# Optimization experiments

Hardware: AMD Instinct MI355X
Metric: run time of the kernel (lower is better)

Reference implementation:

```python
import jax, jax.numpy as jnp
import numpy as np

MAX_HOPS = 2
N_NODES = 100000
N_EDGES = 1600000
D_FEAT = 64

def setup_inputs() -> dict:
    key = jax.random.key(0)
    k1, k2 = jax.random.split(key)
    x = jax.random.normal(k1, (N_NODES, D_FEAT), dtype=jnp.float32)
    edge_index = jax.random.randint(k2, (2, N_EDGES), 0, N_NODES, dtype=jnp.int64)
    hop_weights = jnp.ones((MAX_HOPS + 1,), dtype=jnp.float32)
    return {"x": x, "edge_index": edge_index, "hop_weights": hop_weights}

def reference(x, edge_index, hop_weights):
    num_nodes = x.shape[0]
    loops = jnp.arange(num_nodes, dtype=edge_index.dtype)
    row = jnp.concatenate([edge_index[0], loops])  # destination of scatter-add
    col = jnp.concatenate([edge_index[1], loops])  # gather source
    # symmetric GCN normalization D^{-1/2} A D^{-1/2} (degree computed over col, as in source)
    deg = jax.ops.segment_sum(jnp.ones_like(col, dtype=x.dtype), col, num_segments=num_nodes)
    deg_inv_sqrt = jnp.where(deg > 0, jax.lax.rsqrt(deg), 0.0)
    norm = deg_inv_sqrt[row] * deg_inv_sqrt[col]  # [E+N]
    w = jax.nn.softmax(hop_weights)
    result = w[0] * x
    current = x
    for hop in range(1, MAX_HOPS + 1):
        messages = current[col] * norm[:, None]  # irregular gather + scale
        current = jax.ops.segment_sum(messages, row, num_segments=num_nodes)  # scatter-add
        result = result + w[hop] * current
    return result
```

## Files before the change

### kernel.cpp

```cpp
#include <hip/hip_runtime.h>

#define NN 100000
#define NE 1600000
#define D 64

#define BKT 256
#define BROWS ((NN + BKT - 1) / BKT)
#define CAP 8192
#define PADCAP 8192
#define P1_NB 512
#define P1_T 1024
#define EPB ((NE + P1_NB - 1) / P1_NB)

typedef unsigned short u16;
typedef unsigned int u32;
typedef unsigned char u8;
typedef __attribute__((ext_vector_type(8))) unsigned short us8;


__device__ __forceinline__ float bf2f(u16 u) {
    union { u32 i; float f; } x; x.i = ((u32)u) << 16; return x.f;
}
__device__ __forceinline__ u16 f2bf(float f) {
    union { float f; u32 i; } x; x.f = f;
    u32 r = x.i + 0x7FFF + ((x.i >> 16) & 1);
    return (u16)(r >> 16);
}

__global__ void softmax_kernel(const float* __restrict__ hw, float* __restrict__ wsm) {
    float m = fmaxf(fmaxf(hw[0], hw[1]), hw[2]);
    float e0 = expf(hw[0] - m), e1 = expf(hw[1] - m), e2 = expf(hw[2] - m);
    float s = e0 + e1 + e2;
    wsm[0] = e0 / s; wsm[1] = e1 / s; wsm[2] = e2 / s;
}

__global__ void __launch_bounds__(P1_T) fused_p1(const int* __restrict__ row,
                                                 const int* __restrict__ col,
                                                 int* __restrict__ bcnt,
                                                 int* __restrict__ bcnt2,
                                                 u32* __restrict__ buck,
                                                 u16* __restrict__ buck2) {
    __shared__ int lds_r[EPB];
    __shared__ int lds_c[EPB];
    __shared__ u32 st1[EPB];
    __shared__ u16 st2[EPB];
    __shared__ u8  sb1[EPB];
    __shared__ u8  sb2[EPB];
    __shared__ int h[BKT], h2[BKT];
    __shared__ int hoff[BKT], hoff2[BKT];
    __shared__ int resv[BKT], resv2[BKT];
    int t = threadIdx.x;
    int beg = blockIdx.x * EPB, end = min(NE, beg + EPB);
    int n = end - beg;
    for (int i = t; i < BKT; i += P1_T) { h[i] = 0; h2[i] = 0; }
    __syncthreads();
    for (int i = t; i < n; i += P1_T) {
        int r = row[beg + i], c = col[beg + i];
        lds_r[i] = r; lds_c[i] = c;
        atomicAdd(&h[r / BROWS], 1);
        atomicAdd(&h2[c / BROWS], 1);
    }
    __syncthreads();
    int id = t & 255;
    int side = t >> 8;
    int* arr = (side == 0) ? h : h2;
    int myc = (side < 2) ? arr[id] : 0;
    for (int st = 1; st < BKT; st <<= 1) {
        int u = 0;
        if (side < 2 && id >= st) u = arr[id - st];
        __syncthreads();
        if (side < 2) arr[id] += u;
        __syncthreads();
    }
    if (side == 0) {
        hoff[id] = h[id] - myc;
        resv[id] = atomicAdd(&bcnt[id], myc);
    } else if (side == 1) {
        hoff2[id] = h2[id] - myc;
        resv2[id] = atomicAdd(&bcnt2[id], myc);
    }
    __syncthreads();
    if (t < BKT) h[t] = hoff[t];
    else if (t < 2 * BKT) h2[t - BKT] = hoff2[t - BKT];
    __syncthreads();
    for (int i = t; i < n; i += P1_T) {
        int r = lds_r[i], c = lds_c[i];
        int b1 = r / BROWS;
        int pos = atomicAdd(&h[b1], 1);
        st1[pos] = ((u32)(r - b1 * BROWS) << 17) | (u32)c;
        sb1[pos] = (u8)b1;
        int b2 = c / BROWS;
        int pos2 = atomicAdd(&h2[b2], 1);
        st2[pos2] = (u16)(c - b2 * BROWS);
        sb2[pos2] = (u8)b2;
    }
    __syncthreads();
    for (int i = t; i < n; i += P1_T) {
        int b1 = sb1[i];
        buck[(size_t)b1 * CAP + resv[b1] + (i - hoff[b1])] = st1[i];
        int b2 = sb2[i];
        buck2[(size_t)b2 * CAP + resv2[b2] + (i - hoff2[b2])] = st2[i];
    }
}

__global__ void __launch_bounds__(1024) deg_count(const int* __restrict__ bcnt2,
                                                  const u16* __restrict__ buck2,
                                                  float* __restrict__ dis,
                                                  float* __restrict__ dsi) {
    __shared__ int ca[BROWS];
    int b = blockIdx.x, t = threadIdx.x;
    int row0 = b * BROWS;
    int nrows = min(BROWS, NN - row0);
    int cntb = bcnt2[b];
    const u16* eb = buck2 + (size_t)b * CAP;
    for (int i = t; i < nrows; i += 1024) ca[i] = 0;
    __syncthreads();
    for (int e = t; e < cntb; e += 1024)
        atomicAdd(&ca[eb[e]], 1);
    __syncthreads();
    if (t < nrows) {
        float dg = (float)(ca[t] + 1);
        dis[row0 + t] = rsqrtf(dg);
        dsi[row0 + t] = sqrtf(dg);
    }
}

__global__ void scale_kernel(const float4* __restrict__ x, const float* __restrict__ dis,
                             ushort4* __restrict__ y1, ushort4* __restrict__ y2) {
    int idx = blockIdx.x * blockDim.x + threadIdx.x;
    if (idx >= (NN + 1) * (D / 4)) return;
    if (idx >= NN * (D / 4)) {
        ushort4 z = {0, 0, 0, 0};
        y1[idx] = z; y2[idx] = z;
        return;
    }
    float s = dis[idx >> 4];
    float4 v = x[idx];
    ushort4 o;
    o.x = f2bf(s * v.x); o.y = f2bf(s * v.y); o.z = f2bf(s * v.z); o.w = f2bf(s * v.w);
    y1[idx] = o;
}

__global__ void __launch_bounds__(1024) p2_build(const int* __restrict__ bcnt,
                                                 const u32* __restrict__ buck,
                                                 int* __restrict__ adjc,
                                                 int2* __restrict__ rowbe) {
    __shared__ int ca[BROWS];
    __shared__ int wsum[16];
    int b = blockIdx.x, t = threadIdx.x;
    int row0 = b * BROWS;
    int nrows = min(BROWS, NN - row0);
    int cntb = bcnt[b];
    const u32* eb = buck + (size_t)b * CAP;

    for (int i = t; i < nrows; i += 1024) ca[i] = 0;
    __syncthreads();
    for (int e = t; e < cntb; e += 1024)
        atomicAdd(&ca[eb[e] >> 17], 1);
    __syncthreads();
    int v = (t < nrows) ? ca[t] : 0;
    int vp = (v + 3) & ~3;
    int lane = t & 63, wv = t >> 6;
    int incl = vp;
    #pragma unroll
    for (int d = 1; d < 64; d <<= 1) {
        int u = __shfl_up(incl, d);
        if (lane >= d) incl += u;
    }
    if (lane == 63) wsum[wv] = incl;
    __syncthreads();
    if (t < 16) {
        int s = wsum[t];
        #pragma unroll
        for (int d = 1; d < 16; d <<= 1) {
            int u = __shfl_up(s, d, 16);
            if (t >= d) s += u;
        }
        wsum[t] = s;
    }
    __syncthreads();
    int excl = ((wv > 0) ? wsum[wv - 1] : 0) + incl - vp;
    if (t < nrows) {
        int base = b * PADCAP + excl;
        rowbe[row0 + t] = make_int2(base, base + vp);
        for (int p = base + v; p < base + vp; ++p) adjc[p] = NN;
        ca[t] = base;
    }
    __syncthreads();
    for (int e = t; e < cntb; e += 1024) {
        u32 p = eb[e];
        int pos = atomicAdd(&ca[p >> 17], 1);
        adjc[pos] = (int)(p & 0x1FFFFu);
    }
}


__global__ void prop1_kernel(const int2* __restrict__ rowbe,
                             const int* __restrict__ adjc,
                             const float* __restrict__ dis,
                             const u16* __restrict__ y1,
                             u16* __restrict__ y2) {
    int tid = blockIdx.x * blockDim.x + threadIdx.x;
    int w = tid >> 6, l = tid & 63;
    int half = l >> 5;
    int n = 2 * w + half;
    int sg = (l >> 3) & 3;
    int ho = l & 7;
    int2 be = rowbe[n];
    int j = be.x, end = be.y;
    float a[8] = {0.f, 0.f, 0.f, 0.f, 0.f, 0.f, 0.f, 0.f};
    while (j + 32 <= end) {
        int4 c0 = *(const int4*)&adjc[j + sg * 4];
        int4 c1 = *(const int4*)&adjc[j + 16 + sg * 4];
        us8 v0 = *(const us8*)&y1[c0.x * D + ho * 8];
        us8 v1 = *(const us8*)&y1[c0.y * D + ho * 8];
        us8 v2 = *(const us8*)&y1[c0.z * D + ho * 8];
        us8 v3 = *(const us8*)&y1[c0.w * D + ho * 8];
        us8 v4 = *(const us8*)&y1[c1.x * D + ho * 8];
        us8 v5 = *(const us8*)&y1[c1.y * D + ho * 8];
        us8 v6 = *(const us8*)&y1[c1.z * D + ho * 8];
        us8 v7 = *(const us8*)&y1[c1.w * D + ho * 8];
        #pragma unroll
        for (int k = 0; k < 8; ++k)
            a[k] += ((bf2f(v0[k]) + bf2f(v1[k])) + (bf2f(v2[k]) + bf2f(v3[k])))
                  + ((bf2f(v4[k]) + bf2f(v5[k])) + (bf2f(v6[k]) + bf2f(v7[k])));
        j += 32;
    }
    if (j + 16 <= end) {
        int4 c0 = *(const int4*)&adjc[j + sg * 4];
        us8 v0 = *(const us8*)&y1[c0.x * D + ho * 8];
        us8 v1 = *(const us8*)&y1[c0.y * D + ho * 8];
        us8 v2 = *(const us8*)&y1[c0.z * D + ho * 8];
        us8 v3 = *(const us8*)&y1[c0.w * D + ho * 8];
        #pragma unroll
        for (int k = 0; k < 8; ++k)
            a[k] += (bf2f(v0[k]) + bf2f(v1[k])) + (bf2f(v2[k]) + bf2f(v3[k]));
        j += 16;
    }
    while (j + 4 <= end) {
        int c = adjc[j + sg];
        us8 v0 = *(const us8*)&y1[c * D + ho * 8];
        #pragma unroll
        for (int k = 0; k < 8; ++k) a[k] += bf2f(v0[k]);
        j += 4;
    }
    #pragma unroll
    for (int k = 0; k < 8; ++k) {
        a[k] += __shfl_xor(a[k], 8);
        a[k] += __shfl_xor(a[k], 16);
    }
    if ((l & 31) < 8) {
        us8 s = *(const us8*)&y1[n * D + ho * 8];
        float di = dis[n], d2 = di * di;
        us8 o;
        #pragma unroll
        for (int k = 0; k < 8; ++k) o[k] = f2bf(d2 * (a[k] + bf2f(s[k])));
        *(us8*)&y2[n * D + ho * 8] = o;
    }
}

__global__ void prop2_kernel(const float* __restrict__ x,
                             const int2* __restrict__ rowbe,
                             const int* __restrict__ adjc,
                             const float* __restrict__ dis,
                             const float* __restrict__ dsi,
                             const u16* __restrict__ y2,
                             const float* __restrict__ wsm,
                             float* __restrict__ out) {
    int tid = blockIdx.x * blockDim.x + threadIdx.x;
    int w = tid >> 6, l = tid & 63;
    int half = l >> 5;
    int n = 2 * w + half;
    int sg = (l >> 3) & 3;
    int ho = l & 7;
    int2 be = rowbe[n];
    int j = be.x, end = be.y;
    float a[8] = {0.f, 0.f, 0.f, 0.f, 0.f, 0.f, 0.f, 0.f};
    while (j + 32 <= end) {
        int4 c0 = *(const int4*)&adjc[j + sg * 4];
        int4 c1 = *(const int4*)&adjc[j + 16 + sg * 4];
        us8 v0 = *(const us8*)&y2[c0.x * D + ho * 8];
        us8 v1 = *(const us8*)&y2[c0.y * D + ho * 8];
        us8 v2 = *(const us8*)&y2[c0.z * D + ho * 8];
        us8 v3 = *(const us8*)&y2[c0.w * D + ho * 8];
        us8 v4 = *(const us8*)&y2[c1.x * D + ho * 8];
        us8 v5 = *(const us8*)&y2[c1.y * D + ho * 8];
        us8 v6 = *(const us8*)&y2[c1.z * D + ho * 8];
        us8 v7 = *(const us8*)&y2[c1.w * D + ho * 8];
        #pragma unroll
        for (int k = 0; k < 8; ++k)
            a[k] += ((bf2f(v0[k]) + bf2f(v1[k])) + (bf2f(v2[k]) + bf2f(v3[k])))
                  + ((bf2f(v4[k]) + bf2f(v5[k])) + (bf2f(v6[k]) + bf2f(v7[k])));
        j += 32;
    }
    if (j + 16 <= end) {
        int4 c0 = *(const int4*)&adjc[j + sg * 4];
        us8 v0 = *(const us8*)&y2[c0.x * D + ho * 8];
        us8 v1 = *(const us8*)&y2[c0.y * D + ho * 8];
        us8 v2 = *(const us8*)&y2[c0.z * D + ho * 8];
        us8 v3 = *(const us8*)&y2[c0.w * D + ho * 8];
        #pragma unroll
        for (int k = 0; k < 8; ++k)
            a[k] += (bf2f(v0[k]) + bf2f(v1[k])) + (bf2f(v2[k]) + bf2f(v3[k]));
        j += 16;
    }
    while (j + 4 <= end) {
        int c = adjc[j + sg];
        us8 v0 = *(const us8*)&y2[c * D + ho * 8];
        #pragma unroll
        for (int k = 0; k < 8; ++k) a[k] += bf2f(v0[k]);
        j += 4;
    }
    #pragma unroll
    for (int k = 0; k < 8; ++k) {
        a[k] += __shfl_xor(a[k], 8);
        a[k] += __shfl_xor(a[k], 16);
    }
    if ((l & 31) < 8) {
        us8 s = *(const us8*)&y2[n * D + ho * 8];
        float yk[8];
        #pragma unroll
        for (int k = 0; k < 8; ++k) { yk[k] = bf2f(s[k]); a[k] += yk[k]; }
        float di = dis[n], ds = dsi[n];
        float w0 = wsm[0], w1 = wsm[1], w2 = wsm[2];
        float4 xv0 = *(const float4*)&x[n * D + ho * 8];
        float4 xv1 = *(const float4*)&x[n * D + ho * 8 + 4];
        float4 o0, o1;
        o0.x = w0 * xv0.x + w1 * (ds * yk[0]) + w2 * (di * a[0]);
        o0.y = w0 * xv0.y + w1 * (ds * yk[1]) + w2 * (di * a[1]);
        o0.z = w0 * xv0.z + w1 * (ds * yk[2]) + w2 * (di * a[2]);
        o0.w = w0 * xv0.w + w1 * (ds * yk[3]) + w2 * (di * a[3]);
        o1.x = w0 * xv1.x + w1 * (ds * yk[4]) + w2 * (di * a[4]);
        o1.y = w0 * xv1.y + w1 * (ds * yk[5]) + w2 * (di * a[5]);
        o1.z = w0 * xv1.z + w1 * (ds * yk[6]) + w2 * (di * a[6]);
        o1.w = w0 * xv1.w + w1 * (ds * yk[7]) + w2 * (di * a[7]);
        *(float4*)&out[n * D + ho * 8] = o0;
        *(float4*)&out[n * D + ho * 8 + 4] = o1;
    }
}


extern "C" void kernel_launch(void* const* d_in, const int* in_sizes, int n_in,
                              void* d_out, int out_size, void* d_ws, size_t ws_size,
                              hipStream_t stream) {
    const float* x   = (const float*)d_in[0];
    const int*   ei  = (const int*)d_in[1];
    const float* hw  = (const float*)d_in[2];
    float*       out = (float*)d_out;

    const int* row = ei;
    const int* col = ei + NE;

    char* ws = (char*)d_ws;
    size_t off = 0;
    auto alloc = [&](size_t bytes) { size_t p = off; off += (bytes + 255) & ~(size_t)255; return p; };
    float* wsm    = (float*)(ws + alloc(16));
    int*   bcnt   = (int*)  (ws + alloc((size_t)BKT * 4));
    int*   bcnt2  = (int*)  (ws + alloc((size_t)BKT * 4));
    float* dis    = (float*)(ws + alloc((size_t)NN * 4));
    float* dsi    = (float*)(ws + alloc((size_t)NN * 4));
    u32*   buck   = (u32*)  (ws + alloc((size_t)BKT * CAP * 4));
    u16*   buck2  = (u16*)  (ws + alloc((size_t)BKT * CAP * 2));
    int*   adjc   = (int*)  (ws + alloc((size_t)BKT * PADCAP * 4));
    int2*  rowbe  = (int2*) (ws + alloc((size_t)NN * 8));
    u16*   y1     = (u16*)  (ws + alloc((size_t)(NN + 1) * D * 2));
    u16*   y2     = (u16*)  (ws + alloc((size_t)(NN + 1) * D * 2));

    hipMemsetAsync(bcnt, 0, (size_t)BKT * 4, stream);
    hipMemsetAsync(bcnt2, 0, (size_t)BKT * 4, stream);

    fused_p1<<<P1_NB, P1_T, 0, stream>>>(row, col, bcnt, bcnt2, buck, buck2);
    deg_count<<<BKT, 1024, 0, stream>>>(bcnt2, buck2, dis, dsi);
    softmax_kernel<<<1, 1, 0, stream>>>(hw, wsm);
    scale_kernel<<<((NN + 1) * (D / 4) + 255) / 256, 256, 0, stream>>>(
        (const float4*)x, dis, (ushort4*)y1, (ushort4*)y2);
    p2_build<<<BKT, 1024, 0, stream>>>(bcnt, buck, adjc, rowbe);

    const int prop_blocks = (NN / 2 + 3) / 4;
    prop1_kernel<<<prop_blocks, 256, 0, stream>>>(rowbe, adjc, dis, y1, y2);
    prop2_kernel<<<prop_blocks, 256, 0, stream>>>(x, rowbe, adjc, dis, dsi, y2, wsm, out);
}
```

Before: 126.7 us.

## Fuse setup and scale kernels, pad adjacency rows to 16 for simpler gather loops

Replaces the two memsets and the softmax launch with one setup kernel, and folds the bf16 scaling of x into the degree-count kernel, removing a launch and a reread of dis. Adjacency rows are padded to multiples of 16, pointing at a zero sentinel row, so the propagation loops become a single 16-wide loop with no tail cases. The final combine reads the bf16 y1 instead of the fp32 x, multiplying back by sqrt(deg) to recover it. This cuts traffic and launches, at the cost of extra padded gathers and bf16 rounding of the w0*x term.

```diff
diff --git a/kernel.cpp b/kernel.cpp
--- a/kernel.cpp
+++ b/kernel.cpp
@@ -7,7 +7,7 @@
 #define BKT 256
 #define BROWS ((NN + BKT - 1) / BKT)
 #define CAP 8192
-#define PADCAP 8192
+#define PADCAP 12288
 #define P1_NB 512
 #define P1_T 1024
 #define EPB ((NE + P1_NB - 1) / P1_NB)
@@ -27,11 +27,17 @@
     return (u16)(r >> 16);
 }
 
-__global__ void softmax_kernel(const float* __restrict__ hw, float* __restrict__ wsm) {
-    float m = fmaxf(fmaxf(hw[0], hw[1]), hw[2]);
-    float e0 = expf(hw[0] - m), e1 = expf(hw[1] - m), e2 = expf(hw[2] - m);
-    float s = e0 + e1 + e2;
-    wsm[0] = e0 / s; wsm[1] = e1 / s; wsm[2] = e2 / s;
+__global__ void setup_kernel(const float* __restrict__ hw, float* __restrict__ wsm,
+                             int* __restrict__ bcnt, int* __restrict__ bcnt2) {
+    int t = threadIdx.x;
+    if (t < BKT) bcnt[t] = 0;
+    else if (t < 2 * BKT) bcnt2[t - BKT] = 0;
+    else if (t == 2 * BKT) {
+        float m = fmaxf(fmaxf(hw[0], hw[1]), hw[2]);
+        float e0 = expf(hw[0] - m), e1 = expf(hw[1] - m), e2 = expf(hw[2] - m);
+        float s = e0 + e1 + e2;
+        wsm[0] = e0 / s; wsm[1] = e1 / s; wsm[2] = e2 / s;
+    }
 }
 
 __global__ void __launch_bounds__(P1_T) fused_p1(const int* __restrict__ row,
@@ -103,10 +109,13 @@
     }
 }
 
-__global__ void __launch_bounds__(1024) deg_count(const int* __restrict__ bcnt2,
+__global__ void __launch_bounds__(1024) deg_scale(const int* __restrict__ bcnt2,
                                                   const u16* __restrict__ buck2,
                                                   float* __restrict__ dis,
-                                                  float* __restrict__ dsi) {
+                                                  float* __restrict__ dsi,
+                                                  const float4* __restrict__ x,
+                                                  ushort4* __restrict__ y1,
+                                                  ushort4* __restrict__ y2) {
     __shared__ int ca[BROWS];
     int b = blockIdx.x, t = threadIdx.x;
     int row0 = b * BROWS;
@@ -123,22 +132,21 @@
         dis[row0 + t] = rsqrtf(dg);
         dsi[row0 + t] = sqrtf(dg);
     }
-}
-
-__global__ void scale_kernel(const float4* __restrict__ x, const float* __restrict__ dis,
-                             ushort4* __restrict__ y1, ushort4* __restrict__ y2) {
-    int idx = blockIdx.x * blockDim.x + threadIdx.x;
-    if (idx >= (NN + 1) * (D / 4)) return;
-    if (idx >= NN * (D / 4)) {
+    int items = nrows * 16;
+    for (int i = t; i < items; i += 1024) {
+        int r = i >> 4;
+        float s = rsqrtf((float)(ca[r] + 1));
+        int gidx = (row0 + r) * 16 + (i & 15);
+        float4 v = x[gidx];
+        ushort4 o;
+        o.x = f2bf(s * v.x); o.y = f2bf(s * v.y); o.z = f2bf(s * v.z); o.w = f2bf(s * v.w);
+        y1[gidx] = o;
+    }
+    if (b == BKT - 1 && t < 16) {
         ushort4 z = {0, 0, 0, 0};
-        y1[idx] = z; y2[idx] = z;
-        return;
-    }
-    float s = dis[idx >> 4];
-    float4 v = x[idx];
-    ushort4 o;
-    o.x = f2bf(s * v.x); o.y = f2bf(s * v.y); o.z = f2bf(s * v.z); o.w = f2bf(s * v.w);
-    y1[idx] = o;
+        y1[NN * 16 + t] = z;
+        y2[NN * 16 + t] = z;
+    }
 }
 
 __global__ void __launch_bounds__(1024) p2_build(const int* __restrict__ bcnt,
@@ -159,7 +167,7 @@
         atomicAdd(&ca[eb[e] >> 17], 1);
     __syncthreads();
     int v = (t < nrows) ? ca[t] : 0;
-    int vp = (v + 3) & ~3;
+    int vp = (v + 15) & ~15;
     int lane = t & 63, wv = t >> 6;
     int incl = vp;
     #pragma unroll
@@ -202,47 +210,21 @@
                              u16* __restrict__ y2) {
     int tid = blockIdx.x * blockDim.x + threadIdx.x;
     int w = tid >> 6, l = tid & 63;
-    int half = l >> 5;
-    int n = 2 * w + half;
+    int n = 2 * w + (l >> 5);
     int sg = (l >> 3) & 3;
     int ho = l & 7;
     int2 be = rowbe[n];
-    int j = be.x, end = be.y;
     float a[8] = {0.f, 0.f, 0.f, 0.f, 0.f, 0.f, 0.f, 0.f};
-    while (j + 32 <= end) {
-        int4 c0 = *(const int4*)&adjc[j + sg * 4];
-        int4 c1 = *(const int4*)&adjc[j + 16 + sg * 4];
-        us8 v0 = *(const us8*)&y1[c0.x * D + ho * 8];
-        us8 v1 = *(const us8*)&y1[c0.y * D + ho * 8];
-        us8 v2 = *(const us8*)&y1[c0.z * D + ho * 8];
-        us8 v3 = *(const us8*)&y1[c0.w * D + ho * 8];
-        us8 v4 = *(const us8*)&y1[c1.x * D + ho * 8];
-        us8 v5 = *(const us8*)&y1[c1.y * D + ho * 8];
-        us8 v6 = *(const us8*)&y1[c1.z * D + ho * 8];
-        us8 v7 = *(const us8*)&y1[c1.w * D + ho * 8];
-        #pragma unroll
-        for (int k = 0; k < 8; ++k)
-            a[k] += ((bf2f(v0[k]) + bf2f(v1[k])) + (bf2f(v2[k]) + bf2f(v3[k])))
-                  + ((bf2f(v4[k]) + bf2f(v5[k])) + (bf2f(v6[k]) + bf2f(v7[k])));
-        j += 32;
-    }
-    if (j + 16 <= end) {
-        int4 c0 = *(const int4*)&adjc[j + sg * 4];
-        us8 v0 = *(const us8*)&y1[c0.x * D + ho * 8];
-        us8 v1 = *(const us8*)&y1[c0.y * D + ho * 8];
-        us8 v2 = *(const us8*)&y1[c0.z * D + ho * 8];
-        us8 v3 = *(const us8*)&y1[c0.w * D + ho * 8];
+    #pragma unroll 2
+    for (int j = be.x; j < be.y; j += 16) {
+        int4 c = *(const int4*)&adjc[j + sg * 4];
+        us8 v0 = *(const us8*)&y1[c.x * D + ho * 8];
+        us8 v1 = *(const us8*)&y1[c.y * D + ho * 8];
+        us8 v2 = *(const us8*)&y1[c.z * D + ho * 8];
+        us8 v3 = *(const us8*)&y1[c.w * D + ho * 8];
         #pragma unroll
         for (int k = 0; k < 8; ++k)
             a[k] += (bf2f(v0[k]) + bf2f(v1[k])) + (bf2f(v2[k]) + bf2f(v3[k]));
-        j += 16;
-    }
-    while (j + 4 <= end) {
-        int c = adjc[j + sg];
-        us8 v0 = *(const us8*)&y1[c * D + ho * 8];
-        #pragma unroll
-        for (int k = 0; k < 8; ++k) a[k] += bf2f(v0[k]);
-        j += 4;
     }
     #pragma unroll
     for (int k = 0; k < 8; ++k) {
@@ -259,57 +241,31 @@
     }
 }
 
-__global__ void prop2_kernel(const float* __restrict__ x,
-                             const int2* __restrict__ rowbe,
+__global__ void prop2_kernel(const int2* __restrict__ rowbe,
                              const int* __restrict__ adjc,
                              const float* __restrict__ dis,
                              const float* __restrict__ dsi,
+                             const u16* __restrict__ y1,
                              const u16* __restrict__ y2,
                              const float* __restrict__ wsm,
                              float* __restrict__ out) {
     int tid = blockIdx.x * blockDim.x + threadIdx.x;
     int w = tid >> 6, l = tid & 63;
-    int half = l >> 5;
-    int n = 2 * w + half;
+    int n = 2 * w + (l >> 5);
     int sg = (l >> 3) & 3;
     int ho = l & 7;
     int2 be = rowbe[n];
-    int j = be.x, end = be.y;
     float a[8] = {0.f, 0.f, 0.f, 0.f, 0.f, 0.f, 0.f, 0.f};
-    while (j + 32 <= end) {
-        int4 c0 = *(const int4*)&adjc[j + sg * 4];
-        int4 c1 = *(const int4*)&adjc[j + 16 + sg * 4];
-        us8 v0 = *(const us8*)&y2[c0.x * D + ho * 8];
-        us8 v1 = *(const us8*)&y2[c0.y * D + ho * 8];
-        us8 v2 = *(const us8*)&y2[c0.z * D + ho * 8];
-        us8 v3 = *(const us8*)&y2[c0.w * D + ho * 8];
-        us8 v4 = *(const us8*)&y2[c1.x * D + ho * 8];
-        us8 v5 = *(const us8*)&y2[c1.y * D + ho * 8];
-        us8 v6 = *(const us8*)&y2[c1.z * D + ho * 8];
-        us8 v7 = *(const us8*)&y2[c1.w * D + ho * 8];
-        #pragma unroll
-        for (int k = 0; k < 8; ++k)
-            a[k] += ((bf2f(v0[k]) + bf2f(v1[k])) + (bf2f(v2[k]) + bf2f(v3[k])))
-                  + ((bf2f(v4[k]) + bf2f(v5[k])) + (bf2f(v6[k]) + bf2f(v7[k])));
-        j += 32;
-    }
-    if (j + 16 <= end) {
-        int4 c0 = *(const int4*)&adjc[j + sg * 4];
-        us8 v0 = *(const us8*)&y2[c0.x * D + ho * 8];
-        us8 v1 = *(const us8*)&y2[c0.y * D + ho * 8];
-        us8 v2 = *(const us8*)&y2[c0.z * D + ho * 8];
-        us8 v3 = *(const us8*)&y2[c0.w * D + ho * 8];
+    #pragma unroll 2
+    for (int j = be.x; j < be.y; j += 16) {
+        int4 c = *(const int4*)&adjc[j + sg * 4];
+        us8 v0 = *(const us8*)&y2[c.x * D + ho * 8];
+        us8 v1 = *(const us8*)&y2[c.y * D + ho * 8];
+        us8 v2 = *(const us8*)&y2[c.z * D + ho * 8];
+        us8 v3 = *(const us8*)&y2[c.w * D + ho * 8];
         #pragma unroll
         for (int k = 0; k < 8; ++k)
             a[k] += (bf2f(v0[k]) + bf2f(v1[k])) + (bf2f(v2[k]) + bf2f(v3[k]));
-        j += 16;
-    }
-    while (j + 4 <= end) {
-        int c = adjc[j + sg];
-        us8 v0 = *(const us8*)&y2[c * D + ho * 8];
-        #pragma unroll
-        for (int k = 0; k < 8; ++k) a[k] += bf2f(v0[k]);
-        j += 4;
     }
     #pragma unroll
     for (int k = 0; k < 8; ++k) {
@@ -317,23 +273,18 @@
         a[k] += __shfl_xor(a[k], 16);
     }
     if ((l & 31) < 8) {
-        us8 s = *(const us8*)&y2[n * D + ho * 8];
-        float yk[8];
-        #pragma unroll
-        for (int k = 0; k < 8; ++k) { yk[k] = bf2f(s[k]); a[k] += yk[k]; }
+        us8 s1 = *(const us8*)&y1[n * D + ho * 8];
+        us8 s2 = *(const us8*)&y2[n * D + ho * 8];
         float di = dis[n], ds = dsi[n];
         float w0 = wsm[0], w1 = wsm[1], w2 = wsm[2];
-        float4 xv0 = *(const float4*)&x[n * D + ho * 8];
-        float4 xv1 = *(const float4*)&x[n * D + ho * 8 + 4];
-        float4 o0, o1;
-        o0.x = w0 * xv0.x + w1 * (ds * yk[0]) + w2 * (di * a[0]);
-        o0.y = w0 * xv0.y + w1 * (ds * yk[1]) + w2 * (di * a[1]);
-        o0.z = w0 * xv0.z + w1 * (ds * yk[2]) + w2 * (di * a[2]);
-        o0.w = w0 * xv0.w + w1 * (ds * yk[3]) + w2 * (di * a[3]);
-        o1.x = w0 * xv1.x + w1 * (ds * yk[4]) + w2 * (di * a[4]);
-        o1.y = w0 * xv1.y + w1 * (ds * yk[5]) + w2 * (di * a[5]);
-        o1.z = w0 * xv1.z + w1 * (ds * yk[6]) + w2 * (di * a[6]);
-        o1.w = w0 * xv1.w + w1 * (ds * yk[7]) + w2 * (di * a[7]);
+        float o[8];
+        #pragma unroll
+        for (int k = 0; k < 8; ++k) {
+            float y2k = bf2f(s2[k]);
+            o[k] = ds * (w0 * bf2f(s1[k]) + w1 * y2k) + w2 * (di * (a[k] + y2k));
+        }
+        float4 o0 = {o[0], o[1], o[2], o[3]};
+        float4 o1 = {o[4], o[5], o[6], o[7]};
         *(float4*)&out[n * D + ho * 8] = o0;
         *(float4*)&out[n * D + ho * 8 + 4] = o1;
     }
@@ -366,17 +317,13 @@
     u16*   y1     = (u16*)  (ws + alloc((size_t)(NN + 1) * D * 2));
     u16*   y2     = (u16*)  (ws + alloc((size_t)(NN + 1) * D * 2));
 
-    hipMemsetAsync(bcnt, 0, (size_t)BKT * 4, stream);
-    hipMemsetAsync(bcnt2, 0, (size_t)BKT * 4, stream);
-
+    setup_kernel<<<1, 1024, 0, stream>>>(hw, wsm, bcnt, bcnt2);
     fused_p1<<<P1_NB, P1_T, 0, stream>>>(row, col, bcnt, bcnt2, buck, buck2);
-    deg_count<<<BKT, 1024, 0, stream>>>(bcnt2, buck2, dis, dsi);
-    softmax_kernel<<<1, 1, 0, stream>>>(hw, wsm);
-    scale_kernel<<<((NN + 1) * (D / 4) + 255) / 256, 256, 0, stream>>>(
-        (const float4*)x, dis, (ushort4*)y1, (ushort4*)y2);
+    deg_scale<<<BKT, 1024, 0, stream>>>(bcnt2, buck2, dis, dsi,
+                                        (const float4*)x, (ushort4*)y1, (ushort4*)y2);
     p2_build<<<BKT, 1024, 0, stream>>>(bcnt, buck, adjc, rowbe);
 
     const int prop_blocks = (NN / 2 + 3) / 4;
     prop1_kernel<<<prop_blocks, 256, 0, stream>>>(rowbe, adjc, dis, y1, y2);
-    prop2_kernel<<<prop_blocks, 256, 0, stream>>>(x, rowbe, adjc, dis, dsi, y2, wsm, out);
-}
+    prop2_kernel<<<prop_blocks, 256, 0, stream>>>(rowbe, adjc, dis, dsi, y1, y2, wsm, out);
+}
```

Measured after the change: 117.0 us. 1.08x faster.
